# Kernel tuning notes

Hardware: AMD Instinct MI355X
Metric: run time of the kernel (lower is better)

## Reference

```python
import jax, jax.numpy as jnp
import numpy as np
from jax import lax

K_RATIO = 0.5  # args['k_ratio'], eval (non-training) branch
K_SIZE = 5     # args['gaussian_smooth']['k_size']
C_SIGMA = 1.0  # args['gaussian_smooth']['c_sigma']


def _gaussian_kernel(k_size=K_SIZE, sigma=C_SIGMA):
    # matches Communication.init_gaussian_filter (note: 2*pi*sigma, not sigma^2, as in source)
    c = k_size // 2
    x, y = np.mgrid[-c:k_size - c, -c:k_size - c]
    g = 1.0 / (2.0 * np.pi * sigma) * np.exp(-(np.square(x) + np.square(y)) / (2.0 * np.square(sigma)))
    return jnp.asarray(g, jnp.float32)[None, None]  # (1,1,k,k) OIHW, bias is zero


def setup_inputs() -> dict:
    key = jax.random.key(0)
    conf = jax.random.normal(jax.random.fold_in(key, 1), (8, 6, 4, 512, 512), jnp.float32)
    warp = jnp.ones((8, 1, 512, 512), jnp.float32)
    return {"confidence_maps": conf, "warp_masks": warp, "gauss_kernel": _gaussian_kernel()}


def reference(confidence_maps, warp_masks, gauss_kernel):
    # confidence_maps: (B, L, C, H, W); warp_masks: (B, 1, H, W); gauss_kernel: (1,1,k,k)
    B, L, C, H, W = confidence_maps.shape
    # sigmoid + max over anchor dim, keepdim -> (B, L, 1, H, W)
    m = jnp.max(jax.nn.sigmoid(confidence_maps), axis=2, keepdims=True)
    m = m * warp_masks[:, None]  # broadcast warp mask over agents
    # frozen gaussian smoothing conv, SAME padding (stride 1, pad (k-1)//2)
    sm = lax.conv_general_dilated(m.reshape(B * L, 1, H, W), gauss_kernel,
                                  window_strides=(1, 1), padding='SAME',
                                  dimension_numbers=('NCHW', 'OIHW', 'NCHW'))
    flat = sm.reshape(B, L, H * W)
    K = int(H * W * K_RATIO)  # static k, eval k_ratio branch
    _, idx = lax.top_k(flat, K)  # (B, L, K)
    mask = jnp.zeros_like(flat).at[
        jnp.arange(B)[:, None, None], jnp.arange(L)[None, :, None], idx
    ].set(1.0)  # scatter ones at top-k positions
    # communication rate computed BEFORE ego mask is forced to 1 (as in source)
    rate = jnp.mean(jnp.sum(mask[:, 1:], axis=(1, 2)) / ((L - 1) * H * W))
    mask = mask.reshape(B, L, H, W).at[:, 0].set(1.0)  # ego agent keeps everything
    return mask.reshape(B * L, 1, H, W), rate
```

## Files before the change

### kernel.cpp

```cpp
#include <hip/hip_runtime.h>


#define NROWSEL 40
#define NPIX    262144
#define KSEL    131072
#define CAND_CAP 512
#define KAPPA    3
#define KSCALE   1048576.0f
#define KMAX     1048575.0f

#define OFF_KEY  0ull
#define OFF_H1   41943040ull
#define OFF_H2   41984000ull
#define OFF_ST   42639360ull
#define OFF_CC   42639680ull
#define OFF_CI   42639840ull
#define OFF_CK   42721760ull
#define META_U32 174200

__device__ __forceinline__ float m_val_f32(const float* __restrict__ confr,
                                           const float* __restrict__ warpr,
                                           int gy, int gx) {
  if (gy < 0 || gy >= 512 || gx < 0 || gx >= 512) return 0.0f;
  int off = gy * 512 + gx;
  float x0 = confr[off];
  float x1 = confr[NPIX + off];
  float x2 = confr[2 * NPIX + off];
  float x3 = confr[3 * NPIX + off];
  float mx = fmaxf(fmaxf(x0, x1), fmaxf(x2, x3));
  float s = 1.0f / (1.0f + expf(-mx));
  return s * warpr[off];
}

__device__ __forceinline__ double m_val(const float* __restrict__ confr,
                                        const float* __restrict__ warpr,
                                        int gy, int gx) {
  if (gy < 0 || gy >= 512 || gx < 0 || gx >= 512) return 0.0;
  int off = gy * 512 + gx;
  float x0 = confr[off];
  float x1 = confr[NPIX + off];
  float x2 = confr[2 * NPIX + off];
  float x3 = confr[3 * NPIX + off];
  float mx = fmaxf(fmaxf(x0, x1), fmaxf(x2, x3));
  double s = 1.0 / (1.0 + exp(-(double)mx));
  return s * (double)warpr[off];
}

__device__ __forceinline__ void scan256(const unsigned* __restrict__ cs,
                                        unsigned cum0, int& bsel,
                                        unsigned& above) {
  unsigned cum = cum0;
  bsel = 0; above = cum0;
  for (int c = 255; c >= 0; --c) {
    if (cum + cs[c] >= (unsigned)KSEL) { bsel = c; above = cum; break; }
    cum += cs[c];
  }
}

__device__ __forceinline__ void scan4096(const unsigned* __restrict__ hs,
                                         unsigned* __restrict__ red,
                                         int tid, unsigned cum0,
                                         int* bsel, unsigned* above) {
  unsigned s = 0;
#pragma unroll 4
  for (int k = 0; k < 16; ++k) s += hs[tid * 16 + k];
  red[tid] = s;
  __syncthreads();
  if (tid == 0) {
    unsigned cum = cum0;
    *bsel = 0; *above = cum0;
    for (int c = 255; c >= 0; --c) {
      if (cum + red[c] >= (unsigned)KSEL) {
        unsigned cc2 = cum;
        for (int k = 15; k >= 0; --k) {
          unsigned hv = hs[c * 16 + k];
          if (cc2 + hv >= (unsigned)KSEL) { *bsel = c * 16 + k; *above = cc2; break; }
          cc2 += hv;
        }
        break;
      }
      cum += red[c];
    }
  }
}

__global__ void ego_fill_kernel(float* __restrict__ out,
                                unsigned* __restrict__ meta) {
  int i = blockIdx.x * 256 + threadIdx.x;
  int b = i >> 16;
  int o4 = i & 65535;
  float4* p = (float4*)(out + (size_t)b * 6u * NPIX) + o4;
  *p = make_float4(1.f, 1.f, 1.f, 1.f);
  if (i < META_U32) meta[i] = 0u;
}

__global__ __launch_bounds__(256) void compute_kernel(
    const float* __restrict__ conf, const float* __restrict__ warp,
    const float* __restrict__ gk, unsigned* __restrict__ keys,
    unsigned* __restrict__ hist1) {
  const int blk = blockIdx.x;
  const int j = blk >> 6;
  const int tile = blk & 63;
  const int ty0 = (tile >> 3) << 6;
  const int tx0 = (tile & 7) << 6;
  const int b = j / 5;
  const int l = j % 5 + 1;
  const int rowg = b * 6 + l;
  const float* confr = conf + (size_t)rowg * 4u * NPIX;
  const float* warpr = warp + (size_t)b * NPIX;

  __shared__ float mt[68][68];
  __shared__ unsigned lh[1024];
  __shared__ float wr[5], wc[5];
  const int tid = threadIdx.x;
  if (tid < 5) {
    wr[tid] = gk[10 + tid];
    wc[tid] = gk[tid * 5 + 2] / gk[12];
  }
  for (int i = tid; i < 1024; i += 256) lh[i] = 0u;

  for (int i = tid; i < 68 * 68; i += 256) {
    int hy = i / 68, hx = i - hy * 68;
    mt[hy][hx] = m_val_f32(confr, warpr, ty0 + hy - 2, tx0 + hx - 2);
  }
  __syncthreads();

  const int txl = tid & 63;
  const int y0 = (tid >> 6) << 4;
  const int cpy = tid & 3;
  unsigned* keyrow = keys + (size_t)j * NPIX;

#define HROW(r) ({ float a_ = mt[(r)][txl] * wr[0];            \
                   a_ = fmaf(wr[1], mt[(r)][txl + 1], a_);     \
                   a_ = fmaf(wr[2], mt[(r)][txl + 2], a_);     \
                   a_ = fmaf(wr[3], mt[(r)][txl + 3], a_);     \
                   fmaf(wr[4], mt[(r)][txl + 4], a_); })

  float h0 = HROW(y0);
  float h1 = HROW(y0 + 1);
  float h2 = HROW(y0 + 2);
  float h3 = HROW(y0 + 3);
  for (int yy = y0; yy < y0 + 16; ++yy) {
    float h4 = HROW(yy + 4);
    float acc = h0 * wc[0];
    acc = fmaf(wc[1], h1, acc);
    acc = fmaf(wc[2], h2, acc);
    acc = fmaf(wc[3], h3, acc);
    acc = fmaf(wc[4], h4, acc);
    unsigned k = (unsigned)fminf(fmaxf(acc * KSCALE, 0.0f), KMAX);
    keyrow[(ty0 + yy) * 512 + (tx0 + txl)] = k;
    atomicAdd(&lh[(k >> 12) * 4 + cpy], 1u);
    h0 = h1; h1 = h2; h2 = h3; h3 = h4;
  }
#undef HROW
  __syncthreads();
  if (tid < 256) {
    unsigned s = lh[tid * 4] + lh[tid * 4 + 1] + lh[tid * 4 + 2] + lh[tid * 4 + 3];
    if (s) atomicAdd(&hist1[j * 256 + tid], s);
  }
}

__global__ __launch_bounds__(256) void hist2_kernel(
    const unsigned* __restrict__ keys, const unsigned* __restrict__ hist1,
    unsigned* __restrict__ hist2) {
  int blk = blockIdx.x;
  int j = blk >> 5, seg = blk & 31;
  __shared__ unsigned hs[256];
  __shared__ unsigned lh[8192];
  __shared__ int s_b1;
  int tid = threadIdx.x;
  hs[tid] = hist1[j * 256 + tid];
  for (int i = tid; i < 8192; i += 256) lh[i] = 0u;
  __syncthreads();
  if (tid == 0) {
    int b1; unsigned A1;
    scan256(hs, 0u, b1, A1);
    s_b1 = b1;
  }
  __syncthreads();
  unsigned ub1 = (unsigned)s_b1;
  const uint4* kp = (const uint4*)(keys + (size_t)j * NPIX + seg * 8192);
  int c = tid & 1;
#pragma unroll
  for (int it = 0; it < 8; ++it) {
    uint4 k4 = kp[tid + it * 256];
    if ((k4.x >> 12) == ub1) atomicAdd(&lh[(k4.x & 4095u) * 2 + c], 1u);
    if ((k4.y >> 12) == ub1) atomicAdd(&lh[(k4.y & 4095u) * 2 + c], 1u);
    if ((k4.z >> 12) == ub1) atomicAdd(&lh[(k4.z & 4095u) * 2 + c], 1u);
    if ((k4.w >> 12) == ub1) atomicAdd(&lh[(k4.w & 4095u) * 2 + c], 1u);
  }
  __syncthreads();
  for (int i = tid; i < 4096; i += 256) {
    unsigned s = lh[i * 2] + lh[i * 2 + 1];
    if (s) atomicAdd(&hist2[j * 4096 + i], s);
  }
}

__global__ __launch_bounds__(256) void mask_gather_kernel(
    const unsigned* __restrict__ keys, const unsigned* __restrict__ hist1,
    const unsigned* __restrict__ hist2, float* __restrict__ out,
    int* __restrict__ st, unsigned* __restrict__ ccount,
    int* __restrict__ cidx, unsigned* __restrict__ ckey) {
  int blk = blockIdx.x;
  int j = blk >> 5, seg = blk & 31;
  int b = j / 5, l = j % 5 + 1;
  int rowg = b * 6 + l;
  __shared__ unsigned hs[4096];
  __shared__ unsigned red[256];
  __shared__ int s_pstar;
  int tid = threadIdx.x;
  hs[tid] = hist1[j * 256 + tid];
  __syncthreads();
  int b1 = 0; unsigned A1 = 0;
  if (tid == 0) scan256(hs, 0u, b1, A1);
  __syncthreads();
  for (int i = tid; i < 4096; i += 256) hs[i] = hist2[j * 4096 + i];
  __syncthreads();
  int b2; unsigned A2;
  scan4096(hs, red, tid, A1, &b2, &A2);
  if (tid == 0) {
    s_pstar = (b1 << 12) | b2;
    if (seg == 0) { st[j * 2] = s_pstar; st[j * 2 + 1] = (int)A2; }
  }
  __syncthreads();
  int pstar = s_pstar;

  const uint4* kp = (const uint4*)(keys + (size_t)j * NPIX + seg * 8192);
  float4* o4 = (float4*)(out + (size_t)rowg * NPIX + seg * 8192);
#pragma unroll
  for (int it = 0; it < 8; ++it) {
    int q = tid + it * 256;
    uint4 k4 = kp[q];
    unsigned w[4] = {k4.x, k4.y, k4.z, k4.w};
    float4 mv;
    float* mf = (float*)&mv;
#pragma unroll
    for (int e = 0; e < 4; ++e) {
      int k = (int)w[e];
      mf[e] = k > pstar + KAPPA ? 1.f : 0.f;
      if (k >= pstar - KAPPA && k <= pstar + KAPPA) {
        unsigned s = atomicAdd(&ccount[j], 1u);
        if (s < CAND_CAP) {
          cidx[j * CAND_CAP + s] = seg * 8192 + q * 4 + e;
          ckey[j * CAND_CAP + s] = (unsigned)k;
        }
      }
    }
    o4[q] = mv;
  }
}

__global__ __launch_bounds__(256) void resolve_kernel(
    const float* __restrict__ conf, const float* __restrict__ warp,
    const float* __restrict__ gk, const int* __restrict__ st,
    const unsigned* __restrict__ ccount, const int* __restrict__ cidx,
    const unsigned* __restrict__ ckey, float* __restrict__ out) {
  int j = blockIdx.x;
  int b = j / 5, l = j % 5 + 1;
  int rowg = b * 6 + l;
  const float* confr = conf + (size_t)rowg * 4u * NPIX;
  const float* warpr = warp + (size_t)b * NPIX;
  __shared__ double vs[CAND_CAP];
  __shared__ int ids[CAND_CAP];
  __shared__ unsigned red[256];
  __shared__ double g[25];
  int tid = threadIdx.x;
  if (tid < 25) g[tid] = (double)gk[tid];
  int pstar = st[j * 2];
  int A2 = st[j * 2 + 1];
  int C = (int)min(ccount[j], (unsigned)CAND_CAP);
  __syncthreads();
  unsigned cnt = 0;
  for (int i = tid; i < C; i += 256) {
    int idx = cidx[j * CAND_CAP + i];
    cnt += (int)ckey[j * CAND_CAP + i] > pstar ? 1u : 0u;
    int y = idx >> 9, x = idx & 511;
    double acc = 0.0;
#pragma unroll
    for (int dy = 0; dy < 5; ++dy)
#pragma unroll
      for (int dx = 0; dx < 5; ++dx)
        acc = fma(g[dy * 5 + dx], m_val(confr, warpr, y + dy - 2, x + dx - 2), acc);
    vs[i] = acc;
    ids[i] = idx;
  }
  red[tid] = cnt;
  __syncthreads();
  for (int s = 128; s > 0; s >>= 1) {
    if (tid < s) red[tid] += red[tid + s];
    __syncthreads();
  }
  int R = KSEL - A2 + (int)red[0];
  for (int i = tid; i < C; i += 256) {
    double vi = vs[i];
    int ii = ids[i];
    int rank = 0;
    for (int q = 0; q < C; ++q) {
      double vq = vs[q];
      rank += (vq > vi) || (vq == vi && ids[q] < ii) ? 1 : 0;
    }
    if (rank < R) out[(size_t)rowg * NPIX + ii] = 1.0f;
  }
  if (j == 0 && tid == 0) out[12582912] = 0.5f;
}

extern "C" void kernel_launch(void* const* d_in, const int* in_sizes, int n_in,
                              void* d_out, int out_size, void* d_ws, size_t ws_size,
                              hipStream_t stream) {
  const float* conf = (const float*)d_in[0];
  const float* warp = (const float*)d_in[1];
  const float* gk   = (const float*)d_in[2];
  float* out = (float*)d_out;
  char* ws = (char*)d_ws;

  unsigned* keys = (unsigned*)(ws + OFF_KEY);
  unsigned* h1   = (unsigned*)(ws + OFF_H1);
  unsigned* h2   = (unsigned*)(ws + OFF_H2);
  int*      st   = (int*)(ws + OFF_ST);
  unsigned* cc   = (unsigned*)(ws + OFF_CC);
  int*      ci   = (int*)(ws + OFF_CI);
  unsigned* ck   = (unsigned*)(ws + OFF_CK);

  ego_fill_kernel<<<2048, 256, 0, stream>>>(out, h1);
  compute_kernel<<<NROWSEL * 64, 256, 0, stream>>>(conf, warp, gk, keys, h1);
  hist2_kernel<<<NROWSEL * 32, 256, 0, stream>>>(keys, h1, h2);
  mask_gather_kernel<<<NROWSEL * 32, 256, 0, stream>>>(keys, h1, h2, out, st, cc, ci, ck);
  resolve_kernel<<<NROWSEL, 256, 0, stream>>>(conf, warp, gk, st, cc, ci, ck, out);
}
```

Before: 155.6 us.

## Split sigmoid-max map into separate vectorized kernel before convolution

Computes the sigmoid-max-times-warp map in a standalone float4-vectorized kernel and writes it to a new workspace buffer. The convolution kernel then reads the precomputed map with halo instead of recomputing four conf loads and an exp for every halo pixel. This removes the redundant halo recomputation and gets coalesced vector loads, at the cost of an extra 40 MB write and read through memory and an additional launch. The row loop in the convolution is also forced not to unroll.

```diff
diff --git a/kernel.cpp b/kernel.cpp
--- a/kernel.cpp
+++ b/kernel.cpp
@@ -9,28 +9,15 @@
 #define KSCALE   1048576.0f
 #define KMAX     1048575.0f
 
-#define OFF_KEY  0ull
-#define OFF_H1   41943040ull
-#define OFF_H2   41984000ull
-#define OFF_ST   42639360ull
-#define OFF_CC   42639680ull
-#define OFF_CI   42639840ull
-#define OFF_CK   42721760ull
+#define OFF_M    0ull
+#define OFF_KEY  41943040ull
+#define OFF_H1   83886080ull
+#define OFF_H2   83927040ull
+#define OFF_ST   84582400ull
+#define OFF_CC   84582720ull
+#define OFF_CI   84582880ull
+#define OFF_CK   84664800ull
 #define META_U32 174200
-
-__device__ __forceinline__ float m_val_f32(const float* __restrict__ confr,
-                                           const float* __restrict__ warpr,
-                                           int gy, int gx) {
-  if (gy < 0 || gy >= 512 || gx < 0 || gx >= 512) return 0.0f;
-  int off = gy * 512 + gx;
-  float x0 = confr[off];
-  float x1 = confr[NPIX + off];
-  float x2 = confr[2 * NPIX + off];
-  float x3 = confr[3 * NPIX + off];
-  float mx = fmaxf(fmaxf(x0, x1), fmaxf(x2, x3));
-  float s = 1.0f / (1.0f + expf(-mx));
-  return s * warpr[off];
-}
 
 __device__ __forceinline__ double m_val(const float* __restrict__ confr,
                                         const float* __restrict__ warpr,
@@ -94,20 +81,44 @@
   if (i < META_U32) meta[i] = 0u;
 }
 
-__global__ __launch_bounds__(256) void compute_kernel(
+__global__ __launch_bounds__(256) void m_kernel(
     const float* __restrict__ conf, const float* __restrict__ warp,
-    const float* __restrict__ gk, unsigned* __restrict__ keys,
-    unsigned* __restrict__ hist1) {
+    float* __restrict__ m) {
+  int t = blockIdx.x * 256 + threadIdx.x;
+  for (int it = 0; it < 4; ++it) {
+    int idx = t + it * 655360;
+    int j = idx >> 16;
+    int o = idx & 65535;
+    int b = j / 5, l = j % 5 + 1;
+    const float4* c0 = (const float4*)(conf + ((size_t)(b * 6 + l) * 4u) * NPIX) + o;
+    float4 x0 = c0[0];
+    float4 x1 = c0[65536];
+    float4 x2 = c0[131072];
+    float4 x3 = c0[196608];
+    float4 w  = ((const float4*)(warp + (size_t)b * NPIX))[o];
+    float4 r;
+    float mx;
+    mx = fmaxf(fmaxf(x0.x, x1.x), fmaxf(x2.x, x3.x));
+    r.x = w.x / (1.0f + expf(-mx));
+    mx = fmaxf(fmaxf(x0.y, x1.y), fmaxf(x2.y, x3.y));
+    r.y = w.y / (1.0f + expf(-mx));
+    mx = fmaxf(fmaxf(x0.z, x1.z), fmaxf(x2.z, x3.z));
+    r.z = w.z / (1.0f + expf(-mx));
+    mx = fmaxf(fmaxf(x0.w, x1.w), fmaxf(x2.w, x3.w));
+    r.w = w.w / (1.0f + expf(-mx));
+    ((float4*)(m + (size_t)j * NPIX))[o] = r;
+  }
+}
+
+__global__ __launch_bounds__(256) void conv_kernel(
+    const float* __restrict__ m, const float* __restrict__ gk,
+    unsigned* __restrict__ keys, unsigned* __restrict__ hist1) {
   const int blk = blockIdx.x;
   const int j = blk >> 6;
   const int tile = blk & 63;
   const int ty0 = (tile >> 3) << 6;
   const int tx0 = (tile & 7) << 6;
-  const int b = j / 5;
-  const int l = j % 5 + 1;
-  const int rowg = b * 6 + l;
-  const float* confr = conf + (size_t)rowg * 4u * NPIX;
-  const float* warpr = warp + (size_t)b * NPIX;
+  const float* mr = m + (size_t)j * NPIX;
 
   __shared__ float mt[68][68];
   __shared__ unsigned lh[1024];
@@ -121,7 +132,10 @@
 
   for (int i = tid; i < 68 * 68; i += 256) {
     int hy = i / 68, hx = i - hy * 68;
-    mt[hy][hx] = m_val_f32(confr, warpr, ty0 + hy - 2, tx0 + hx - 2);
+    int gy = ty0 + hy - 2, gx = tx0 + hx - 2;
+    float v = 0.0f;
+    if (gy >= 0 && gy < 512 && gx >= 0 && gx < 512) v = mr[gy * 512 + gx];
+    mt[hy][hx] = v;
   }
   __syncthreads();
 
@@ -140,6 +154,7 @@
   float h1 = HROW(y0 + 1);
   float h2 = HROW(y0 + 2);
   float h3 = HROW(y0 + 3);
+#pragma unroll 1
   for (int yy = y0; yy < y0 + 16; ++yy) {
     float h4 = HROW(yy + 4);
     float acc = h0 * wc[0];
@@ -313,6 +328,7 @@
   float* out = (float*)d_out;
   char* ws = (char*)d_ws;
 
+  float*    mArr = (float*)(ws + OFF_M);
   unsigned* keys = (unsigned*)(ws + OFF_KEY);
   unsigned* h1   = (unsigned*)(ws + OFF_H1);
   unsigned* h2   = (unsigned*)(ws + OFF_H2);
@@ -322,7 +338,8 @@
   unsigned* ck   = (unsigned*)(ws + OFF_CK);
 
   ego_fill_kernel<<<2048, 256, 0, stream>>>(out, h1);
-  compute_kernel<<<NROWSEL * 64, 256, 0, stream>>>(conf, warp, gk, keys, h1);
+  m_kernel<<<2560, 256, 0, stream>>>(conf, warp, mArr);
+  conv_kernel<<<NROWSEL * 64, 256, 0, stream>>>(mArr, gk, keys, h1);
   hist2_kernel<<<NROWSEL * 32, 256, 0, stream>>>(keys, h1, h2);
   mask_gather_kernel<<<NROWSEL * 32, 256, 0, stream>>>(keys, h1, h2, out, st, cc, ci, ck);
   resolve_kernel<<<NROWSEL, 256, 0, stream>>>(conf, warp, gk, st, cc, ci, ck, out);
```

Result: no change. 157.6 us (+1.3%).
